# Kernel optimization log

Measured on AMD Instinct MI355X. Metric: run time of the kernel, lower is better.

Reference implementation:

```python
import jax, jax.numpy as jnp
import numpy as np

PROPAGATION_RANGE = 2
PROP_OUT = PROPAGATION_RANGE - 1  # propagation_out_range


def setup_inputs() -> dict:
    key = jax.random.key(0)
    k1, k2 = jax.random.split(key)
    B, D, H, W = 2, 48, 512, 640
    neighbors = 9
    depth_min = jnp.full((B,), 425.0, dtype=jnp.float32)
    depth_max = jnp.full((B,), 935.0, dtype=jnp.float32)
    # depth samples uniformly inside [depth_min, depth_max]
    u = jax.random.uniform(k1, (B, D, H, W), dtype=jnp.float32)
    depth_sample = depth_min[:, None, None, None] + u * (depth_max - depth_min)[:, None, None, None]
    # per-neighbor weights (2*neighbors channels: far-range then near-range)
    offset = jax.random.uniform(k2, (B, 2 * neighbors, H, W), dtype=jnp.float32) / neighbors
    return {
        "depth_sample": depth_sample,
        "depth_min": depth_min,
        "depth_max": depth_max,
        "offset": offset,
        "patchmatch_interval_scale": 0.025,
        "evaluate_neighbors": neighbors,
    }


def reference(depth_sample, depth_min, depth_max, offset, patchmatch_interval_scale, evaluate_neighbors):
    neighbors = int(evaluate_neighbors)
    B, D, H, W = depth_sample.shape
    k = int(np.sqrt(neighbors))  # square neighborhood side

    # normalized inverse depth in [0, 1]
    inv_min = 1.0 / depth_min  # [B]
    inv_max = 1.0 / depth_max  # [B]
    x = (1.0 / depth_sample - inv_max[:, None, None, None]) / (inv_min - inv_max)[:, None, None, None]

    pad = k // 2 + PROP_OUT
    pad1 = 2 * pad
    xp = jnp.pad(x, ((0, 0), (0, 0), (pad, pad), (pad, pad)), mode="reflect")
    xp1 = jnp.pad(x, ((0, 0), (0, 0), (pad1, pad1), (pad1, pad1)), mode="reflect")

    step = PROP_OUT + 1
    acc = jnp.zeros_like(x)
    for s in range(neighbors):  # small static loop (9 neighbors)
        iy, ix = (s // k) * step, (s % k) * step
        iy1, ix1 = 2 * iy, 2 * ix
        # offset channel broadcasts over the depth dimension
        f1 = offset[:, s, None] * xp1[:, :, iy1:H + iy1, ix1:W + ix1]
        f = offset[:, s + neighbors, None] * xp[:, :, iy:H + iy, ix:W + ix]
        acc = acc + (f + f1) * 0.5

    x1 = jnp.abs(acc - x) / patchmatch_interval_scale
    x1 = jnp.clip(x1, 0.0, 4.0)
    return jax.nn.sigmoid((2.0 - x1) * 2.0)
```

## Files before the change

### kernel.cpp

```cpp
#include <hip/hip_runtime.h>

constexpr int Bc = 2, Dc = 48, Hc = 512, Wc = 640;
constexpr int HWc = Hc * Wc;

constexpr int TW = 32, TH = 16, NT = 256;
constexpr int NXT = Wc / TW;
constexpr int NYT = Hc / TH;
constexpr int NBLK = NXT * NYT * Bc;
constexpr int NXCD = 8;
constexpr int BPX = NBLK / NXCD;
constexpr int HALO = 4;
constexpr int SW = TW + 2 * HALO;
constexpr int SH = TH + 2 * HALO;
constexpr int PLANE = SW * SH;
constexpr int DC = 2;
constexpr int NIT = Dc / DC;
constexpr int NVEC = DC * PLANE / 4;
constexpr int VPT = (NVEC + NT - 1) / NT;
constexpr int NSC = DC * PLANE;
constexpr int SPT = (NSC + NT - 1) / NT;

__device__ __forceinline__ int reflect_h(int h) {
    return h < 0 ? -h : (h >= Hc ? 2 * (Hc - 1) - h : h);
}
__device__ __forceinline__ int reflect_w(int w) {
    return w < 0 ? -w : (w >= Wc ? 2 * (Wc - 1) - w : w);
}

__global__ __launch_bounds__(NT) void dw_kernel(
    const float* __restrict__ ds, const float* __restrict__ dmin,
    const float* __restrict__ dmax, const float* __restrict__ off,
    const float* __restrict__ scale_p, float* __restrict__ out)
{
    __shared__ float sx[2][DC * PLANE];

    const int hw  = blockIdx.x;
    const int l   = (hw & (NXCD - 1)) * BPX + (hw >> 3);
    const int bx  = l % NXT;
    const int rem = l / NXT;
    const int by  = rem % NYT;
    const int b   = rem / NYT;
    const int h0  = by * TH;
    const int w0  = bx * TW;
    const int tid = threadIdx.x;
    const int col = tid & 15;
    const int row = tid >> 4;

    const float inv_min   = 1.0f / dmin[b];
    const float inv_max   = 1.0f / dmax[b];
    const float invd      = 1.0f / (inv_min - inv_max);
    const float inv_scale = 1.0f / scale_p[0];

    float offF[9][2], offN[9][2];
    {
        const float* op = off + (size_t)b * 18 * HWc
                        + (size_t)(h0 + row) * Wc + (w0 + 2 * col);
        #pragma unroll
        for (int s = 0; s < 9; ++s) {
            float2 vF = *(const float2*)(op + (size_t)s * HWc);
            float2 vN = *(const float2*)(op + (size_t)(s + 9) * HWc);
            offF[s][0] = vF.x; offF[s][1] = vF.y;
            offN[s][0] = vN.x; offN[s][1] = vN.y;
        }
    }

    const float* dsb  = ds  + (size_t)b * Dc * HWc;
    float*       outb = out + (size_t)b * Dc * HWc
                            + (size_t)(h0 + row) * Wc + (w0 + 2 * col);

    auto compute = [&](const float* sb, int d0) {
        #pragma unroll
        for (int p = 0; p < DC; ++p) {
            const float* bp = sb + p * PLANE + (row + HALO) * SW + (HALO + 2 * col);
            float a0 = 0.f, a1 = 0.f, x00, x01;
            float2 t0, t1, t2, t3, t4;
            t0 = *(const float2*)(bp - 4 * SW - 4);
            t1 = *(const float2*)(bp - 4 * SW);
            t2 = *(const float2*)(bp - 4 * SW + 4);
            a0 += offF[0][0]*t0.x + offF[1][0]*t1.x + offF[2][0]*t2.x;
            a1 += offF[0][1]*t0.y + offF[1][1]*t1.y + offF[2][1]*t2.y;
            t0 = *(const float2*)(bp - 2 * SW - 2);
            t1 = *(const float2*)(bp - 2 * SW);
            t2 = *(const float2*)(bp - 2 * SW + 2);
            a0 += offN[0][0]*t0.x + offN[1][0]*t1.x + offN[2][0]*t2.x;
            a1 += offN[0][1]*t0.y + offN[1][1]*t1.y + offN[2][1]*t2.y;
            t0 = *(const float2*)(bp - 4);
            t1 = *(const float2*)(bp - 2);
            t2 = *(const float2*)(bp);
            t3 = *(const float2*)(bp + 2);
            t4 = *(const float2*)(bp + 4);
            x00 = t2.x; x01 = t2.y;
            a0 += offN[3][0]*t1.x + offN[4][0]*t2.x + offN[5][0]*t3.x
                + offF[3][0]*t0.x + offF[4][0]*t2.x + offF[5][0]*t4.x;
            a1 += offN[3][1]*t1.y + offN[4][1]*t2.y + offN[5][1]*t3.y
                + offF[3][1]*t0.y + offF[4][1]*t2.y + offF[5][1]*t4.y;
            t0 = *(const float2*)(bp + 2 * SW - 2);
            t1 = *(const float2*)(bp + 2 * SW);
            t2 = *(const float2*)(bp + 2 * SW + 2);
            a0 += offN[6][0]*t0.x + offN[7][0]*t1.x + offN[8][0]*t2.x;
            a1 += offN[6][1]*t0.y + offN[7][1]*t1.y + offN[8][1]*t2.y;
            t0 = *(const float2*)(bp + 4 * SW - 4);
            t1 = *(const float2*)(bp + 4 * SW);
            t2 = *(const float2*)(bp + 4 * SW + 4);
            a0 += offF[6][0]*t0.x + offF[7][0]*t1.x + offF[8][0]*t2.x;
            a1 += offF[6][1]*t0.y + offF[7][1]*t1.y + offF[8][1]*t2.y;
            float2 o;
            a0 *= 0.5f; a1 *= 0.5f;
            float x1a = fminf(fabsf(a0 - x00) * inv_scale, 4.0f);
            float x1b = fminf(fabsf(a1 - x01) * inv_scale, 4.0f);
            o.x = __builtin_amdgcn_rcpf(1.0f + __expf(-(4.0f - 2.0f * x1a)));
            o.y = __builtin_amdgcn_rcpf(1.0f + __expf(-(4.0f - 2.0f * x1b)));
            *(float2*)(outb + (size_t)(d0 + p) * HWc) = o;
        }
    };

    const bool interior = (bx > 0) && (bx + 1 < NXT);

    if (interior) {
        int vsrc[VPT];
        #pragma unroll
        for (int i = 0; i < VPT; ++i) {
            int vid = tid + i * NT;
            if (vid < NVEC) {
                int p   = vid / (PLANE / 4);
                int rem2 = vid - p * (PLANE / 4);
                int r   = rem2 / (SW / 4);
                int j   = rem2 - r * (SW / 4);
                int hs  = reflect_h(h0 + r - HALO);
                vsrc[i] = p * HWc + hs * Wc + (w0 - HALO + 4 * j);
            } else vsrc[i] = 0;
        }
        float4 pre[VPT];
        auto issue = [&](int d0) {
            const float* dp = dsb + (size_t)d0 * HWc;
            #pragma unroll
            for (int i = 0; i < VPT; ++i) {
                int vid = tid + i * NT;
                if (vid < NVEC) pre[i] = *(const float4*)(dp + vsrc[i]);
            }
        };
        auto commit = [&](float* sb) {
            #pragma unroll
            for (int i = 0; i < VPT; ++i) {
                int vid = tid + i * NT;
                if (vid < NVEC) {
                    float4 v = pre[i], x;
                    x.x = (__builtin_amdgcn_rcpf(v.x) - inv_max) * invd;
                    x.y = (__builtin_amdgcn_rcpf(v.y) - inv_max) * invd;
                    x.z = (__builtin_amdgcn_rcpf(v.z) - inv_max) * invd;
                    x.w = (__builtin_amdgcn_rcpf(v.w) - inv_max) * invd;
                    *(float4*)(sb + vid * 4) = x;
                }
            }
        };
        issue(0);
        commit(sx[0]);
        __syncthreads();
        for (int it = 0; it < NIT; ++it) {
            if (it + 1 < NIT) issue((it + 1) * DC);
            compute(sx[it & 1], it * DC);
            if (it + 1 < NIT) commit(sx[(it + 1) & 1]);
            __syncthreads();
        }
    } else {
        int ssrc[SPT];
        #pragma unroll
        for (int i = 0; i < SPT; ++i) {
            int idx = tid + i * NT;
            if (idx < NSC) {
                int p   = idx / PLANE;
                int rem2 = idx - p * PLANE;
                int r   = rem2 / SW;
                int c   = rem2 - r * SW;
                int hs  = reflect_h(h0 + r - HALO);
                int ws  = reflect_w(w0 + c - HALO);
                ssrc[i] = p * HWc + hs * Wc + ws;
            } else ssrc[i] = 0;
        }
        float pre[SPT];
        auto issue = [&](int d0) {
            const float* dp = dsb + (size_t)d0 * HWc;
            #pragma unroll
            for (int i = 0; i < SPT; ++i) {
                int idx = tid + i * NT;
                if (idx < NSC) pre[i] = dp[ssrc[i]];
            }
        };
        auto commit = [&](float* sb) {
            #pragma unroll
            for (int i = 0; i < SPT; ++i) {
                int idx = tid + i * NT;
                if (idx < NSC)
                    sb[idx] = (__builtin_amdgcn_rcpf(pre[i]) - inv_max) * invd;
            }
        };
        issue(0);
        commit(sx[0]);
        __syncthreads();
        for (int it = 0; it < NIT; ++it) {
            if (it + 1 < NIT) issue((it + 1) * DC);
            compute(sx[it & 1], it * DC);
            if (it + 1 < NIT) commit(sx[(it + 1) & 1]);
            __syncthreads();
        }
    }
}

extern "C" void kernel_launch(void* const* d_in, const int* in_sizes, int n_in,
                              void* d_out, int out_size, void* d_ws, size_t ws_size,
                              hipStream_t stream) {
    const float* ds   = (const float*)d_in[0];
    const float* dmin = (const float*)d_in[1];
    const float* dmax = (const float*)d_in[2];
    const float* off  = (const float*)d_in[3];
    const float* sc   = (const float*)d_in[4];
    float* out = (float*)d_out;

    dim3 grid(NBLK, 1, 1);
    dw_kernel<<<grid, NT, 0, stream>>>(ds, dmin, dmax, off, sc, out);
}
```

Before: 271.6 us.

## Stage four depth planes per iteration and drop register prefetch on border tiles

Doubles the depth chunk per shared-memory stage from two to four planes, halving the number of barriers and iterations while doubling the LDS footprint per block. Border tiles no longer precompute and hold gather addresses and a prefetch buffer in registers; they recompute reflected addresses and load, convert and store in batches of eight after compute, which gives up load/compute overlap there to reduce register pressure. The 0.5 averaging factor is folded into the offset weights and the inverse-depth normalisation becomes a single fma. Larger LDS use per block may reduce occupancy.

```diff
diff --git a/kernel.cpp b/kernel.cpp
--- a/kernel.cpp
+++ b/kernel.cpp
@@ -13,12 +13,12 @@
 constexpr int SW = TW + 2 * HALO;
 constexpr int SH = TH + 2 * HALO;
 constexpr int PLANE = SW * SH;
-constexpr int DC = 2;
+constexpr int DC = 4;
 constexpr int NIT = Dc / DC;
 constexpr int NVEC = DC * PLANE / 4;
 constexpr int VPT = (NVEC + NT - 1) / NT;
 constexpr int NSC = DC * PLANE;
-constexpr int SPT = (NSC + NT - 1) / NT;
+constexpr int SPT = NSC / NT;
 
 __device__ __forceinline__ int reflect_h(int h) {
     return h < 0 ? -h : (h >= Hc ? 2 * (Hc - 1) - h : h);
@@ -49,6 +49,7 @@
     const float inv_min   = 1.0f / dmin[b];
     const float inv_max   = 1.0f / dmax[b];
     const float invd      = 1.0f / (inv_min - inv_max);
+    const float nmc       = -inv_max * invd;
     const float inv_scale = 1.0f / scale_p[0];
 
     float offF[9][2], offN[9][2];
@@ -59,8 +60,8 @@
         for (int s = 0; s < 9; ++s) {
             float2 vF = *(const float2*)(op + (size_t)s * HWc);
             float2 vN = *(const float2*)(op + (size_t)(s + 9) * HWc);
-            offF[s][0] = vF.x; offF[s][1] = vF.y;
-            offN[s][0] = vN.x; offN[s][1] = vN.y;
+            offF[s][0] = 0.5f * vF.x; offF[s][1] = 0.5f * vF.y;
+            offN[s][0] = 0.5f * vN.x; offN[s][1] = 0.5f * vN.y;
         }
     }
 
@@ -105,7 +106,6 @@
             a0 += offF[6][0]*t0.x + offF[7][0]*t1.x + offF[8][0]*t2.x;
             a1 += offF[6][1]*t0.y + offF[7][1]*t1.y + offF[8][1]*t2.y;
             float2 o;
-            a0 *= 0.5f; a1 *= 0.5f;
             float x1a = fminf(fabsf(a0 - x00) * inv_scale, 4.0f);
             float x1b = fminf(fabsf(a1 - x01) * inv_scale, 4.0f);
             o.x = __builtin_amdgcn_rcpf(1.0f + __expf(-(4.0f - 2.0f * x1a)));
@@ -122,12 +122,12 @@
         for (int i = 0; i < VPT; ++i) {
             int vid = tid + i * NT;
             if (vid < NVEC) {
-                int p   = vid / (PLANE / 4);
+                int p    = vid / (PLANE / 4);
                 int rem2 = vid - p * (PLANE / 4);
-                int r   = rem2 / (SW / 4);
-                int j   = rem2 - r * (SW / 4);
-                int hs  = reflect_h(h0 + r - HALO);
-                vsrc[i] = p * HWc + hs * Wc + (w0 - HALO + 4 * j);
+                int r    = rem2 / (SW / 4);
+                int j    = rem2 - r * (SW / 4);
+                int hs   = reflect_h(h0 + r - HALO);
+                vsrc[i]  = p * HWc + hs * Wc + (w0 - HALO + 4 * j);
             } else vsrc[i] = 0;
         }
         float4 pre[VPT];
@@ -145,10 +145,10 @@
                 int vid = tid + i * NT;
                 if (vid < NVEC) {
                     float4 v = pre[i], x;
-                    x.x = (__builtin_amdgcn_rcpf(v.x) - inv_max) * invd;
-                    x.y = (__builtin_amdgcn_rcpf(v.y) - inv_max) * invd;
-                    x.z = (__builtin_amdgcn_rcpf(v.z) - inv_max) * invd;
-                    x.w = (__builtin_amdgcn_rcpf(v.w) - inv_max) * invd;
+                    x.x = fmaf(__builtin_amdgcn_rcpf(v.x), invd, nmc);
+                    x.y = fmaf(__builtin_amdgcn_rcpf(v.y), invd, nmc);
+                    x.z = fmaf(__builtin_amdgcn_rcpf(v.z), invd, nmc);
+                    x.w = fmaf(__builtin_amdgcn_rcpf(v.w), invd, nmc);
                     *(float4*)(sb + vid * 4) = x;
                 }
             }
@@ -163,44 +163,41 @@
             __syncthreads();
         }
     } else {
-        int ssrc[SPT];
-        #pragma unroll
-        for (int i = 0; i < SPT; ++i) {
-            int idx = tid + i * NT;
-            if (idx < NSC) {
-                int p   = idx / PLANE;
-                int rem2 = idx - p * PLANE;
-                int r   = rem2 / SW;
-                int c   = rem2 - r * SW;
-                int hs  = reflect_h(h0 + r - HALO);
-                int ws  = reflect_w(w0 + c - HALO);
-                ssrc[i] = p * HWc + hs * Wc + ws;
-            } else ssrc[i] = 0;
-        }
-        float pre[SPT];
-        auto issue = [&](int d0) {
+        auto stage_direct = [&](int d0, float* sb) {
             const float* dp = dsb + (size_t)d0 * HWc;
             #pragma unroll
-            for (int i = 0; i < SPT; ++i) {
-                int idx = tid + i * NT;
-                if (idx < NSC) pre[i] = dp[ssrc[i]];
+            for (int c = 0; c < 2; ++c) {
+                const int kn = (c == 0) ? 8 : (SPT - 8);
+                int adr[8]; float val[8];
+                #pragma unroll
+                for (int i = 0; i < 8; ++i) {
+                    if (i < kn) {
+                        int idx  = tid + (c * 8 + i) * NT;
+                        int p    = idx / PLANE;
+                        int rem2 = idx - p * PLANE;
+                        int r    = rem2 / SW;
+                        int cc   = rem2 - r * SW;
+                        int hs   = reflect_h(h0 + r - HALO);
+                        int ws   = reflect_w(w0 + cc - HALO);
+                        adr[i]   = p * HWc + hs * Wc + ws;
+                    }
+                }
+                #pragma unroll
+                for (int i = 0; i < 8; ++i)
+                    if (i < kn) val[i] = dp[adr[i]];
+                #pragma unroll
+                for (int i = 0; i < 8; ++i)
+                    if (i < kn) {
+                        int idx = tid + (c * 8 + i) * NT;
+                        sb[idx] = fmaf(__builtin_amdgcn_rcpf(val[i]), invd, nmc);
+                    }
             }
         };
-        auto commit = [&](float* sb) {
-            #pragma unroll
-            for (int i = 0; i < SPT; ++i) {
-                int idx = tid + i * NT;
-                if (idx < NSC)
-                    sb[idx] = (__builtin_amdgcn_rcpf(pre[i]) - inv_max) * invd;
-            }
-        };
-        issue(0);
-        commit(sx[0]);
+        stage_direct(0, sx[0]);
         __syncthreads();
         for (int it = 0; it < NIT; ++it) {
-            if (it + 1 < NIT) issue((it + 1) * DC);
             compute(sx[it & 1], it * DC);
-            if (it + 1 < NIT) commit(sx[(it + 1) & 1]);
+            if (it + 1 < NIT) stage_direct((it + 1) * DC, sx[(it + 1) & 1]);
             __syncthreads();
         }
     }
```

Measured after the change: 286.8 us. 1.06x slower.
